# Kernel optimization log

Measured on AMD Instinct MI355X. Metric: run time of the kernel, lower is better.

The kernel has to match this reference:

```python
import jax, jax.numpy as jnp
import numpy as np

DIM = 512
HEADS = 8
HEAD_DIM = DIM // HEADS
SCALE = HEAD_DIM ** -0.5
CPB_HIDDEN = 512
N_CLASSES = 2
LN_EPS = 1e-5


def _layernorm(x, g, b):
    m = jnp.mean(x, axis=-1, keepdims=True)
    v = jnp.var(x, axis=-1, keepdims=True)
    return (x - m) / jnp.sqrt(v + LN_EPS) * g + b


def _coord_attention(x, coords, cpb_w1, cpb_b1, cpb_w2, cpb_b2, qkv_w, qkv_b, proj_w, proj_b):
    B, N, C = x.shape
    qkv = (x @ qkv_w + qkv_b).reshape(B, N, 3, HEADS, HEAD_DIM)
    q, k, v = jnp.moveaxis(qkv, 2, 0)  # each (B, N, H, hd)
    attn = jnp.einsum('bnhd,bmhd->bhnm', q * SCALE, k)  # (B, H, N, N)
    rel = coords[:, :, None, :] - coords[:, None, :, :]  # (B, N, N, 2)
    rel = rel / (jnp.linalg.norm(rel, axis=-1, keepdims=True) + 1e-6)
    bias = jax.nn.relu(rel @ cpb_w1 + cpb_b1) @ cpb_w2 + cpb_b2  # (B, N, N, H)
    attn = jax.nn.softmax(attn + jnp.transpose(bias, (0, 3, 1, 2)), axis=-1)
    out = jnp.einsum('bhnm,bmhd->bnhd', attn, v).reshape(B, N, C)
    return out @ proj_w + proj_b


def setup_inputs() -> dict:
    key = jax.random.key(0)
    ks = iter(jax.random.split(key, 32))
    d = {}
    d['h'] = jax.random.normal(next(ks), (1, 400, 1024), dtype=jnp.float32)
    d['coords'] = jax.random.uniform(next(ks), (1, 400, 2), dtype=jnp.float32) * 1000.0
    def lin(kw, kb, fan_in, fan_out):
        w = jax.random.normal(kw, (fan_in, fan_out), dtype=jnp.float32) / np.sqrt(fan_in)
        b = jax.random.normal(kb, (fan_out,), dtype=jnp.float32) * 0.01
        return w, b
    d['fc1_w'], d['fc1_b'] = lin(next(ks), next(ks), 1024, DIM)
    d['cls_token'] = jax.random.normal(next(ks), (1, 1, DIM), dtype=jnp.float32)
    for p in ('l1', 'l2'):
        d[p + '_norm_g'] = jnp.ones((DIM,), jnp.float32)
        d[p + '_norm_b'] = jnp.zeros((DIM,), jnp.float32)
        d[p + '_cpb_w1'], d[p + '_cpb_b1'] = lin(next(ks), next(ks), 2, CPB_HIDDEN)
        d[p + '_cpb_w2'], d[p + '_cpb_b2'] = lin(next(ks), next(ks), CPB_HIDDEN, HEADS)
        d[p + '_qkv_w'], d[p + '_qkv_b'] = lin(next(ks), next(ks), DIM, 3 * DIM)
        d[p + '_proj_w'], d[p + '_proj_b'] = lin(next(ks), next(ks), DIM, DIM)
    d['norm_g'] = jnp.ones((DIM,), jnp.float32)
    d['norm_b'] = jnp.zeros((DIM,), jnp.float32)
    d['fc2_w'], d['fc2_b'] = lin(next(ks), next(ks), DIM, N_CLASSES)
    return d


def reference(h, coords, fc1_w, fc1_b, cls_token,
              l1_norm_g, l1_norm_b, l1_cpb_w1, l1_cpb_b1, l1_cpb_w2, l1_cpb_b2,
              l1_qkv_w, l1_qkv_b, l1_proj_w, l1_proj_b,
              l2_norm_g, l2_norm_b, l2_cpb_w1, l2_cpb_b1, l2_cpb_w2, l2_cpb_b2,
              l2_qkv_w, l2_qkv_b, l2_proj_w, l2_proj_b,
              norm_g, norm_b, fc2_w, fc2_b):
    B, Np, _ = h.shape
    h = jax.nn.relu(h @ fc1_w + fc1_b)  # (B, N, 512)
    side = int(np.ceil(np.sqrt(Np)))
    add = side * side - Np  # pad bag to a perfect square (wrap-around copy)
    h = jnp.concatenate([h, h[:, :add, :]], axis=1)
    coords = jnp.concatenate([coords, coords[:, :add, :]], axis=1)
    cls = jnp.broadcast_to(cls_token, (B, 1, DIM))
    h = jnp.concatenate([cls, h], axis=1)
    coords = jnp.concatenate([jnp.zeros((B, 1, 2), h.dtype), coords], axis=1)
    h = h + _coord_attention(_layernorm(h, l1_norm_g, l1_norm_b), coords,
                             l1_cpb_w1, l1_cpb_b1, l1_cpb_w2, l1_cpb_b2,
                             l1_qkv_w, l1_qkv_b, l1_proj_w, l1_proj_b)
    h = h + _coord_attention(_layernorm(h, l2_norm_g, l2_norm_b), coords,
                             l2_cpb_w1, l2_cpb_b1, l2_cpb_w2, l2_cpb_b2,
                             l2_qkv_w, l2_qkv_b, l2_proj_w, l2_proj_b)
    h = _layernorm(h, norm_g, norm_b)[:, 0]  # CLS token
    return h @ fc2_w + fc2_b  # (B, n_classes)
```

## Files before the change

### kernel.cpp

```cpp
#include <hip/hip_runtime.h>
#include <math.h>

#define NP 401
#define DIM 512
#define LN_EPS 1e-5f
#define ATT_SCALE 0.125f
#define CPB_M 4096
#define TSTRIDE (CPB_M + 64)
#define PQS (401L * 1536)
#define PKS (401L * 1024)
#define PVS (401L * 512)

template<bool TB, typename LA, typename LB>
__device__ __forceinline__ void gemm64(
    int kBeg, int kEnd, int tid,
    float (*as)[68], float (*bs)[68], float (&acc)[4][4],
    LA&& loadA, LB&& loadB)
{
    float aR[4], bR[4];
    loadA(kBeg, aR);
    loadB(kBeg, bR);
    for (int k0 = kBeg; k0 < kEnd; k0 += 16) {
        const int arow = tid >> 2, aq = tid & 3;
        as[aq * 4 + 0][arow] = aR[0];
        as[aq * 4 + 1][arow] = aR[1];
        as[aq * 4 + 2][arow] = aR[2];
        as[aq * 4 + 3][arow] = aR[3];
        if (!TB) {
            *(float4*)&bs[tid >> 4][(tid & 15) * 4] =
                make_float4(bR[0], bR[1], bR[2], bR[3]);
        } else {
            bs[aq * 4 + 0][arow] = bR[0];
            bs[aq * 4 + 1][arow] = bR[1];
            bs[aq * 4 + 2][arow] = bR[2];
            bs[aq * 4 + 3][arow] = bR[3];
        }
        __syncthreads();
        float nA[4] = {0.f,0.f,0.f,0.f}, nB[4] = {0.f,0.f,0.f,0.f};
        if (k0 + 16 < kEnd) { loadA(k0 + 16, nA); loadB(k0 + 16, nB); }
        const int tx = tid & 15, ty = tid >> 4;
        #pragma unroll
        for (int kk = 0; kk < 16; ++kk) {
            float4 a4 = *(const float4*)&as[kk][ty * 4];
            float4 b4 = *(const float4*)&bs[kk][tx * 4];
            float av[4] = {a4.x, a4.y, a4.z, a4.w};
            float bv[4] = {b4.x, b4.y, b4.z, b4.w};
            #pragma unroll
            for (int r = 0; r < 4; ++r)
                #pragma unroll
                for (int c = 0; c < 4; ++c)
                    acc[r][c] = fmaf(av[r], bv[c], acc[r][c]);
        }
        __syncthreads();
        #pragma unroll
        for (int j = 0; j < 4; ++j) { aR[j] = nA[j]; bR[j] = nB[j]; }
    }
}

template<typename LA, typename LB>
__device__ __forceinline__ void gemm256(
    int kBeg, int kEnd, int tid,
    float (*as)[68], float (*bs)[260], float (&acc)[4][4][4],
    LA&& loadA, LB&& loadB)
{
    float aR[4], bR[4][4];
    loadA(kBeg, aR);
    loadB(kBeg, bR);
    for (int k0 = kBeg; k0 < kEnd; k0 += 16) {
        const int arow = tid >> 2, aq = tid & 3;
        as[aq * 4 + 0][arow] = aR[0];
        as[aq * 4 + 1][arow] = aR[1];
        as[aq * 4 + 2][arow] = aR[2];
        as[aq * 4 + 3][arow] = aR[3];
        {
            const int brow = tid >> 4, bcol = (tid & 15) * 4;
            #pragma unroll
            for (int j = 0; j < 4; ++j)
                *(float4*)&bs[brow][bcol + 64 * j] =
                    make_float4(bR[j][0], bR[j][1], bR[j][2], bR[j][3]);
        }
        __syncthreads();
        float nA[4] = {0.f,0.f,0.f,0.f};
        float nB[4][4] = {};
        if (k0 + 16 < kEnd) { loadA(k0 + 16, nA); loadB(k0 + 16, nB); }
        const int tx = tid & 15, ty = tid >> 4;
        #pragma unroll
        for (int kk = 0; kk < 16; ++kk) {
            float4 a4 = *(const float4*)&as[kk][ty * 4];
            float av[4] = {a4.x, a4.y, a4.z, a4.w};
            #pragma unroll
            for (int j = 0; j < 4; ++j) {
                float4 b4 = *(const float4*)&bs[kk][tx * 4 + 64 * j];
                float bv[4] = {b4.x, b4.y, b4.z, b4.w};
                #pragma unroll
                for (int r = 0; r < 4; ++r)
                    #pragma unroll
                    for (int c = 0; c < 4; ++c)
                        acc[r][j][c] = fmaf(av[r], bv[c], acc[r][j][c]);
            }
        }
        __syncthreads();
        #pragma unroll
        for (int i = 0; i < 4; ++i) aR[i] = nA[i];
        #pragma unroll
        for (int j = 0; j < 4; ++j)
            #pragma unroll
            for (int i = 0; i < 4; ++i) bR[j][i] = nB[j][i];
    }
}

__global__ __launch_bounds__(256) void gemm_split256_kernel(
    const float* __restrict__ A, int lda,
    const float* __restrict__ B, int ldb,
    float* __restrict__ P, int ldc, long slice,
    int M, int K, int skN)
{
    __shared__ float as[16][68], bs[16][260];
    const int tid = threadIdx.x;
    const int m0 = blockIdx.x * 64, n0 = blockIdx.y * 256;
    const int sk = blockIdx.z;
    const int KS = K / skN;
    const int kBeg = sk * KS, kEnd = kBeg + KS;
    float acc[4][4][4] = {};

    auto loadA = [&](int k0, float r[4]) {
        r[0] = r[1] = r[2] = r[3] = 0.f;
        int gm = m0 + (tid >> 2);
        if (gm >= M) return;
        int gk = k0 + (tid & 3) * 4;
        float4 v = *(const float4*)(A + (long)gm * lda + gk);
        r[0]=v.x; r[1]=v.y; r[2]=v.z; r[3]=v.w;
    };
    auto loadB = [&](int k0, float r[4][4]) {
        int gk = k0 + (tid >> 4);
        const float* p = B + (long)gk * ldb + n0 + (tid & 15) * 4;
        #pragma unroll
        for (int j = 0; j < 4; ++j) {
            float4 v = *(const float4*)(p + 64 * j);
            r[j][0]=v.x; r[j][1]=v.y; r[j][2]=v.z; r[j][3]=v.w;
        }
    };
    gemm256(kBeg, kEnd, tid, as, bs, acc, loadA, loadB);

    float* C = P + (long)sk * slice;
    const int tx = tid & 15, ty = tid >> 4;
    #pragma unroll
    for (int r = 0; r < 4; ++r) {
        int m = m0 + ty * 4 + r;
        if (m >= M) continue;
        #pragma unroll
        for (int j = 0; j < 4; ++j)
            *(float4*)&C[(long)m * ldc + n0 + tx * 4 + 64 * j] =
                make_float4(acc[r][j][0], acc[r][j][1],
                            acc[r][j][2], acc[r][j][3]);
    }
}

__global__ __launch_bounds__(256) void flash_kernel(
    const float* __restrict__ Pq,
    const float* __restrict__ qkvb,
    const int* __restrict__ pm, const float* __restrict__ pf,
    const float* __restrict__ T,
    float* __restrict__ PO,
    float* __restrict__ Pml)
{
    __shared__ float as[16][68], bs[16][68];
    __shared__ float pT[64][68];
    __shared__ float vs[64][68];
    const int tid = threadIdx.x;
    const int m0 = blockIdx.x * 64, nb = blockIdx.y, h = blockIdx.z;
    const int n0 = nb * 64;
    float acc[4][4] = {};

    float vreg[4][4];
    {
        int key = n0 + (tid >> 2);
        int d0 = (tid & 3) * 16;
        if (key <= 400) {
            long base = (long)key * 1536 + 1024 + h * 64 + d0;
            #pragma unroll
            for (int i = 0; i < 4; ++i) {
                float4 bb = *(const float4*)(qkvb + 1024 + h * 64 + d0 + i * 4);
                float r0 = bb.x, r1 = bb.y, r2 = bb.z, r3 = bb.w;
                #pragma unroll
                for (int s = 0; s < 8; ++s) {
                    float4 v = *(const float4*)(Pq + (long)s * PQS + base + i * 4);
                    r0 += v.x; r1 += v.y; r2 += v.z; r3 += v.w;
                }
                vreg[i][0] = r0; vreg[i][1] = r1;
                vreg[i][2] = r2; vreg[i][3] = r3;
            }
        } else {
            #pragma unroll
            for (int i = 0; i < 4; ++i)
                vreg[i][0] = vreg[i][1] = vreg[i][2] = vreg[i][3] = 0.f;
        }
    }

    auto loadQ = [&](int k0, float r[4]) {
        int gm = m0 + (tid >> 2);
        if (gm > 400) { r[0]=r[1]=r[2]=r[3]=0.f; return; }
        int gk = k0 + (tid & 3) * 4;
        long base = (long)gm * 1536 + h * 64 + gk;
        float4 bb = *(const float4*)(qkvb + h * 64 + gk);
        r[0] = bb.x; r[1] = bb.y; r[2] = bb.z; r[3] = bb.w;
        #pragma unroll
        for (int s = 0; s < 8; ++s) {
            float4 v = *(const float4*)(Pq + (long)s * PQS + base);
            r[0] += v.x; r[1] += v.y; r[2] += v.z; r[3] += v.w;
        }
    };
    auto loadK = [&](int k0, float r[4]) {
        int gn = n0 + (tid >> 2);
        if (gn > 400) { r[0]=r[1]=r[2]=r[3]=0.f; return; }
        int gk = k0 + (tid & 3) * 4;
        long base = (long)gn * 1536 + 512 + h * 64 + gk;
        float4 bb = *(const float4*)(qkvb + 512 + h * 64 + gk);
        r[0] = bb.x; r[1] = bb.y; r[2] = bb.z; r[3] = bb.w;
        #pragma unroll
        for (int s = 0; s < 8; ++s) {
            float4 v = *(const float4*)(Pq + (long)s * PQS + base);
            r[0] += v.x; r[1] += v.y; r[2] += v.z; r[3] += v.w;
        }
    };
    gemm64<true>(0, 64, tid, as, bs, acc, loadQ, loadK);

    {
        int key = tid >> 2, d0 = (tid & 3) * 16;
        #pragma unroll
        for (int i = 0; i < 4; ++i)
            *(float4*)&vs[key][d0 + i * 4] =
                make_float4(vreg[i][0], vreg[i][1], vreg[i][2], vreg[i][3]);
    }

    const int tx = tid & 15, ty = tid >> 4;
    const float* Tt = T + (long)h * TSTRIDE;
    float p[4][4];
    #pragma unroll
    for (int r = 0; r < 4; ++r) {
        int i = m0 + ty * 4 + r;
        float sv[4];
        #pragma unroll
        for (int c = 0; c < 4; ++c) {
            int j = n0 + tx * 4 + c;
            if (i <= 400 && j <= 400) {
                int id = i * 416 + j;
                int mm = pm[id];
                float fr = pf[id];
                float t0 = Tt[mm], t1 = Tt[mm + 1];
                sv[c] = fmaf(acc[r][c], ATT_SCALE, fmaf(fr, t1 - t0, t0));
            } else {
                sv[c] = -INFINITY;
            }
        }
        float cmax = fmaxf(fmaxf(sv[0], sv[1]), fmaxf(sv[2], sv[3]));
        cmax = fmaxf(cmax, __shfl_xor(cmax, 1));
        cmax = fmaxf(cmax, __shfl_xor(cmax, 2));
        cmax = fmaxf(cmax, __shfl_xor(cmax, 4));
        cmax = fmaxf(cmax, __shfl_xor(cmax, 8));
        const bool rowok = (i <= 400);
        #pragma unroll
        for (int c = 0; c < 4; ++c)
            p[r][c] = rowok ? __expf(sv[c] - cmax) : 0.f;
        float cs = p[r][0] + p[r][1] + p[r][2] + p[r][3];
        cs += __shfl_xor(cs, 1);
        cs += __shfl_xor(cs, 2);
        cs += __shfl_xor(cs, 4);
        cs += __shfl_xor(cs, 8);
        if (tx == 0 && rowok) {
            long o = ((long)(h * 401 + i) * 7 + nb) * 2;
            Pml[o] = cmax;
            Pml[o + 1] = cs;
        }
    }
    #pragma unroll
    for (int c = 0; c < 4; ++c)
        *(float4*)&pT[tx * 4 + c][ty * 4] =
            make_float4(p[0][c], p[1][c], p[2][c], p[3][c]);
    __syncthreads();

    float o[4][4] = {};
    #pragma unroll 16
    for (int kk = 0; kk < 64; ++kk) {
        float4 a4 = *(const float4*)&pT[kk][ty * 4];
        float4 b4 = *(const float4*)&vs[kk][tx * 4];
        float av[4] = {a4.x, a4.y, a4.z, a4.w};
        float bv[4] = {b4.x, b4.y, b4.z, b4.w};
        #pragma unroll
        for (int r = 0; r < 4; ++r)
            #pragma unroll
            for (int c = 0; c < 4; ++c)
                o[r][c] = fmaf(av[r], bv[c], o[r][c]);
    }

    float* C = PO + (long)nb * PVS;
    #pragma unroll
    for (int r = 0; r < 4; ++r) {
        int m = m0 + ty * 4 + r;
        if (m > 400) continue;
        *(float4*)&C[(long)m * 512 + h * 64 + tx * 4] =
            make_float4(o[r][0], o[r][1], o[r][2], o[r][3]);
    }
}

__global__ __launch_bounds__(256) void proj_kernel(
    const float* __restrict__ PO, const float* __restrict__ Pml,
    const float* __restrict__ projw, float* __restrict__ Pp)
{
    __shared__ float as[16][68], bs[16][68];
    __shared__ float wls[64][8];
    const int tid = threadIdx.x;
    const int m0 = blockIdx.x * 64, n0 = blockIdx.y * 64, sk = blockIdx.z;
    const int kBeg = sk * 64, kEnd = kBeg + 64;
    float acc[4][4] = {};

    if (tid < 64) {
        int row = m0 + tid;
        if (row <= 400) {
            const float* q = Pml + ((long)(sk * 401 + row) * 7) * 2;
            float M = -INFINITY;
            #pragma unroll
            for (int c = 0; c < 7; ++c) M = fmaxf(M, q[c * 2]);
            float D = 0.f;
            #pragma unroll
            for (int c = 0; c < 7; ++c) D += q[c * 2 + 1] * __expf(q[c * 2] - M);
            float iD = 1.f / D;
            #pragma unroll
            for (int c = 0; c < 7; ++c) wls[tid][c] = __expf(q[c * 2] - M) * iD;
        } else {
            #pragma unroll
            for (int c = 0; c < 7; ++c) wls[tid][c] = 0.f;
        }
    }
    __syncthreads();

    auto loadA = [&](int k0, float r4[4]) {
        r4[0] = r4[1] = r4[2] = r4[3] = 0.f;
        int lm = tid >> 2, gm = m0 + lm;
        if (gm > 400) return;
        int gk = k0 + (tid & 3) * 4;
        #pragma unroll
        for (int s = 0; s < 7; ++s) {
            float4 v = *(const float4*)(PO + (long)s * PVS + (long)gm * 512 + gk);
            float w = wls[lm][s];
            r4[0] = fmaf(w, v.x, r4[0]);
            r4[1] = fmaf(w, v.y, r4[1]);
            r4[2] = fmaf(w, v.z, r4[2]);
            r4[3] = fmaf(w, v.w, r4[3]);
        }
    };
    auto loadB = [&](int k0, float r[4]) {
        int gk = k0 + (tid >> 4);
        int gn = n0 + (tid & 15) * 4;
        float4 v = *(const float4*)(projw + (long)gk * 512 + gn);
        r[0]=v.x; r[1]=v.y; r[2]=v.z; r[3]=v.w;
    };
    gemm64<false>(kBeg, kEnd, tid, as, bs, acc, loadA, loadB);

    float* C = Pp + (long)sk * PVS;
    const int tx = tid & 15, ty = tid >> 4;
    #pragma unroll
    for (int r = 0; r < 4; ++r) {
        int m = m0 + ty * 4 + r;
        if (m > 400) continue;
        *(float4*)&C[(long)m * 512 + n0 + tx * 4] =
            make_float4(acc[r][0], acc[r][1], acc[r][2], acc[r][3]);
    }
}

__global__ __launch_bounds__(256) void rowfuse_kernel(
    const float* __restrict__ P, long slice, int skN, int rowOff,
    const float* __restrict__ bias, int doRelu,
    const float* __restrict__ resid, const float* __restrict__ cls,
    float* __restrict__ h0,
    const float* __restrict__ g, const float* __restrict__ b,
    float* __restrict__ xln)
{
    const int r = blockIdx.x, t = threadIdx.x;
    float v0, v1;
    if (cls && r == 0) {
        v0 = cls[t]; v1 = cls[t + 256];
    } else {
        const float* p = P + (long)(r - rowOff) * DIM;
        v0 = bias[t]; v1 = bias[t + 256];
        for (int k = 0; k < skN; ++k) {
            v0 += p[(long)k * slice + t];
            v1 += p[(long)k * slice + t + 256];
        }
        if (resid) {
            v0 += resid[(long)r * DIM + t];
            v1 += resid[(long)r * DIM + t + 256];
        }
        if (doRelu) { v0 = fmaxf(v0, 0.f); v1 = fmaxf(v1, 0.f); }
    }
    h0[(long)r * DIM + t] = v0;
    h0[(long)r * DIM + t + 256] = v1;

    float s = v0 + v1, sq = v0 * v0 + v1 * v1;
    #pragma unroll
    for (int off = 32; off > 0; off >>= 1) {
        s += __shfl_down(s, off);
        sq += __shfl_down(sq, off);
    }
    __shared__ float ps[4], pq[4];
    int w = t >> 6, lane = t & 63;
    if (lane == 0) { ps[w] = s; pq[w] = sq; }
    __syncthreads();
    float Sm = ps[0] + ps[1] + ps[2] + ps[3];
    float Q = pq[0] + pq[1] + pq[2] + pq[3];
    float mean = Sm * (1.f / DIM);
    float var = Q * (1.f / DIM) - mean * mean;
    float inv = rsqrtf(var + LN_EPS);
    xln[(long)r * DIM + t]       = (v0 - mean) * inv * g[t] + b[t];
    xln[(long)r * DIM + t + 256] = (v1 - mean) * inv * g[t + 256] + b[t + 256];
}

__global__ __launch_bounds__(256) void cls_decode_kernel(
    const float* __restrict__ xln, const float* __restrict__ qkvw,
    const float* __restrict__ Pkv, const float* __restrict__ qkvb,
    const int* __restrict__ pm, const float* __restrict__ pf,
    const float* __restrict__ T,
    float* __restrict__ cms, float* __restrict__ cpv,
    unsigned* __restrict__ cnt)
{
    const int h = blockIdx.x, c = blockIdx.y, tid = threadIdx.x;
    const int kBeg = c * 64;
    __shared__ float q0[64], scraw[64], p[64], red[4][64], rr[2];

    if (h == 0 && c == 0 && tid == 0) *cnt = 0u;

    {
        int d = tid & 63, w4 = tid >> 6;
        const float* col = qkvw + h * 64 + d;
        float acc = 0.f;
        for (int k = w4 * 128; k < w4 * 128 + 128; ++k)
            acc = fmaf(xln[k], col[(long)k * 1536], acc);
        red[w4][d] = acc;
    }
    __syncthreads();
    if (tid < 64)
        q0[tid] = red[0][tid] + red[1][tid] + red[2][tid] + red[3][tid]
                  + qkvb[h * 64 + tid];
    __syncthreads();

    {
        int k = tid >> 2, q = tid & 3;
        int j = kBeg + k;
        float dot = 0.f;
        if (j < NP) {
            long base = (long)j * 1024 + h * 64 + q * 16;
            #pragma unroll
            for (int d = 0; d < 16; d += 4) {
                float4 x = *(const float4*)(qkvb + 512 + h * 64 + q * 16 + d);
                #pragma unroll
                for (int s = 0; s < 8; ++s) {
                    float4 v = *(const float4*)(Pkv + (long)s * PKS + base + d);
                    x.x += v.x; x.y += v.y; x.z += v.z; x.w += v.w;
                }
                float4 qq = *(const float4*)(q0 + q * 16 + d);
                dot = fmaf(qq.x, x.x, dot);
                dot = fmaf(qq.y, x.y, dot);
                dot = fmaf(qq.z, x.z, dot);
                dot = fmaf(qq.w, x.w, dot);
            }
        }
        dot += __shfl_down(dot, 2);
        dot += __shfl_down(dot, 1);
        if (q == 0) scraw[k] = dot;
    }
    __syncthreads();

    if (tid < 64) {
        int j = kBeg + tid;
        float s;
        if (j < NP) {
            int mm = pm[j];
            float fr = pf[j];
            const float* Tt = T + (long)h * TSTRIDE;
            float t0 = Tt[mm], t1 = Tt[mm + 1];
            s = fmaf(scraw[tid], ATT_SCALE, fmaf(fr, t1 - t0, t0));
        } else {
            s = -INFINITY;
        }
        float m = s;
        #pragma unroll
        for (int off = 32; off > 0; off >>= 1)
            m = fmaxf(m, __shfl_xor(m, off));
        float e = (j < NP) ? __expf(s - m) : 0.f;
        float sum = e;
        #pragma unroll
        for (int off = 32; off > 0; off >>= 1)
            sum += __shfl_xor(sum, off);
        p[tid] = e;
        if (tid == 0) { rr[0] = m; rr[1] = sum; }
    }
    __syncthreads();

    {
        int w = tid >> 6, d = tid & 63;
        float vb = qkvb[1024 + h * 64 + d];
        float acc = 0.f;
        for (int k = w; k < 64; k += 4) {
            int j = kBeg + k;
            if (j >= NP) break;
            long o = (long)j * 1024 + 512 + h * 64 + d;
            float v = vb;
            #pragma unroll
            for (int s = 0; s < 8; ++s) v += Pkv[(long)s * PKS + o];
            acc = fmaf(p[k], v, acc);
        }
        red[w][d] = acc;
    }
    __syncthreads();
    if (tid < 64) {
        cpv[((long)h * 7 + c) * 64 + tid] =
            red[0][tid] + red[1][tid] + red[2][tid] + red[3][tid];
        if (tid == 0) {
            cms[(h * 7 + c) * 2 + 0] = rr[0];
            cms[(h * 7 + c) * 2 + 1] = rr[1];
        }
    }
}

__global__ __launch_bounds__(256) void cls_proj_kernel(
    const float* __restrict__ cms, const float* __restrict__ cpv,
    const float* __restrict__ projw, const float* __restrict__ projb,
    float* __restrict__ proj0,
    const float* __restrict__ h0,
    const float* __restrict__ g, const float* __restrict__ b,
    const float* __restrict__ fc2w, const float* __restrict__ fc2b,
    float* __restrict__ out, unsigned* __restrict__ cnt)
{
    __shared__ float av[512], red[4][64];
    __shared__ int isLast;
    const int bk = blockIdx.x, tid = threadIdx.x;
    for (int d = tid; d < 512; d += 256) {
        int h = d >> 6, dd = d & 63;
        float M = -INFINITY;
        #pragma unroll
        for (int c = 0; c < 7; ++c)
            M = fmaxf(M, cms[(h * 7 + c) * 2]);
        float Sx = 0.f, acc = 0.f;
        #pragma unroll
        for (int c = 0; c < 7; ++c) {
            float e = __expf(cms[(h * 7 + c) * 2] - M);
            Sx += cms[(h * 7 + c) * 2 + 1] * e;
            acc += cpv[((long)h * 7 + c) * 64 + dd] * e;
        }
        av[d] = acc / Sx;
    }
    __syncthreads();
    int gg = tid >> 6, n = bk * 64 + (tid & 63);
    float acc = 0.f;
    for (int k = gg * 128; k < gg * 128 + 128; ++k)
        acc = fmaf(av[k], projw[(long)k * 512 + n], acc);
    red[gg][tid & 63] = acc;
    __syncthreads();
    if (tid < 64)
        proj0[bk * 64 + tid] = red[0][tid] + red[1][tid] + red[2][tid]
                               + red[3][tid] + projb[bk * 64 + tid];

    __threadfence();
    if (tid == 0) isLast = (atomicAdd(cnt, 1u) == 7u);
    __syncthreads();
    if (!isLast) return;
    __threadfence();

    const int t = tid;
    float v0 = h0[t] + proj0[t];
    float v1 = h0[t + 256] + proj0[t + 256];
    float s = v0 + v1, sq = v0 * v0 + v1 * v1;
    #pragma unroll
    for (int off = 32; off > 0; off >>= 1) {
        s += __shfl_down(s, off);
        sq += __shfl_down(sq, off);
    }
    __shared__ float ps[4], pq[4], pc0[4], pc1[4];
    int w = t >> 6, lane = t & 63;
    if (lane == 0) { ps[w] = s; pq[w] = sq; }
    __syncthreads();
    float Sm = ps[0] + ps[1] + ps[2] + ps[3];
    float Q = pq[0] + pq[1] + pq[2] + pq[3];
    float mean = Sm * (1.f / DIM);
    float var = Q * (1.f / DIM) - mean * mean;
    float inv = rsqrtf(var + LN_EPS);
    float n0 = (v0 - mean) * inv * g[t] + b[t];
    float n1 = (v1 - mean) * inv * g[t + 256] + b[t + 256];
    float c0 = n0 * fc2w[t * 2]     + n1 * fc2w[(t + 256) * 2];
    float c1 = n0 * fc2w[t * 2 + 1] + n1 * fc2w[(t + 256) * 2 + 1];
    #pragma unroll
    for (int off = 32; off > 0; off >>= 1) {
        c0 += __shfl_down(c0, off);
        c1 += __shfl_down(c1, off);
    }
    if (lane == 0) { pc0[w] = c0; pc1[w] = c1; }
    __syncthreads();
    if (t == 0) {
        out[0] = pc0[0] + pc0[1] + pc0[2] + pc0[3] + fc2b[0];
        out[1] = pc1[0] + pc1[1] + pc1[2] + pc1[3] + fc2b[1];
    }
}

__global__ __launch_bounds__(256) void mega_kernel(
    const float* __restrict__ hin, const float* __restrict__ fc1_w,
    const float* __restrict__ w1_0, const float* __restrict__ b1_0,
    const float* __restrict__ w2_0, const float* __restrict__ b2_0,
    const float* __restrict__ w1_1, const float* __restrict__ b1_1,
    const float* __restrict__ w2_1, const float* __restrict__ b2_1,
    const float* __restrict__ coords,
    float* __restrict__ Pp, float* __restrict__ T,
    int* __restrict__ pm, float* __restrict__ pf)
{
    __shared__ float smem[5248];
    float (*as)[68]  = (float(*)[68])smem;
    float (*bs)[260] = (float(*)[260])(smem + 1088);
    float (*red)[64][8] = (float(*)[64][8])smem;
    const int bid = blockIdx.x, tid = threadIdx.x;

    if (bid < 224) {
        int sk = bid / 14, rem = bid % 14;
        int m0 = (rem % 7) * 64, n0 = (rem / 7) * 256;
        int kBeg = sk * 64, kEnd = kBeg + 64;
        float acc[4][4][4] = {};
        auto loadA = [&](int k0, float r[4]) {
            r[0]=r[1]=r[2]=r[3]=0.f;
            int gm = m0 + (tid >> 2);
            if (gm >= 400) return;
            int gk = k0 + (tid & 3) * 4;
            float4 v = *(const float4*)(hin + (long)gm * 1024 + gk);
            r[0]=v.x; r[1]=v.y; r[2]=v.z; r[3]=v.w;
        };
        auto loadB = [&](int k0, float r[4][4]) {
            int gk = k0 + (tid >> 4);
            const float* p = fc1_w + (long)gk * 512 + n0 + (tid & 15) * 4;
            #pragma unroll
            for (int j = 0; j < 4; ++j) {
                float4 v = *(const float4*)(p + 64 * j);
                r[j][0]=v.x; r[j][1]=v.y; r[j][2]=v.z; r[j][3]=v.w;
            }
        };
        gemm256(kBeg, kEnd, tid, as, bs, acc, loadA, loadB);
        float* C = Pp + (long)sk * PVS;
        const int tx = tid & 15, ty = tid >> 4;
        #pragma unroll
        for (int r = 0; r < 4; ++r) {
            int m = m0 + ty * 4 + r;
            if (m >= 400) continue;
            #pragma unroll
            for (int j = 0; j < 4; ++j)
                *(float4*)&C[(long)m * 512 + n0 + tx * 4 + 64 * j] =
                    make_float4(acc[r][j][0], acc[r][j][1],
                                acc[r][j][2], acc[r][j][3]);
        }
    } else if (bid < 354) {
        int tb = bid - 224;
        int z = tb / 65, ab = tb % 65;
        const float* w1 = z ? w1_1 : w1_0;
        const float* b1 = z ? b1_1 : b1_0;
        const float* w2 = z ? w2_1 : w2_0;
        const float* b2 = z ? b2_1 : b2_0;
        const int lane = tid & 63, wv = tid >> 6;
        float ca = 0.f, sa = 0.f;
        if (ab != 64) {
            float th = fmaf((float)(ab * 64 + lane),
                            (float)(2.0 * M_PI / CPB_M), -(float)M_PI);
            sincosf(th, &sa, &ca);
        } else if (lane == 0) {
            sincosf((float)M_PI, &sa, &ca);
        }
        float a8[8] = {};
        const int kbeg = wv * 128;
        #pragma unroll 4
        for (int k = kbeg; k < kbeg + 128; ++k) {
            float hk = fmaxf(fmaf(ca, w1[k],
                                  fmaf(sa, w1[512 + k], b1[k])), 0.f);
            #pragma unroll
            for (int h2 = 0; h2 < 8; ++h2)
                a8[h2] = fmaf(hk, w2[k * 8 + h2], a8[h2]);
        }
        #pragma unroll
        for (int h2 = 0; h2 < 8; ++h2) red[wv][lane][h2] = a8[h2];
        __syncthreads();
        if (tid < 64) {
            int aidx = ab * 64 + tid;
            if (aidx <= CPB_M + 1) {
                #pragma unroll
                for (int h2 = 0; h2 < 8; ++h2)
                    T[(long)(z * 8 + h2) * TSTRIDE + aidx] =
                        red[0][tid][h2] + red[1][tid][h2] +
                        red[2][tid][h2] + red[3][tid][h2] + b2[h2];
            }
        }
    } else {
        int p = (bid - 354) * 256 + tid;
        if (p < NP * NP) {
            int i = p / NP, j = p - i * NP;
            float xi = (i == 0) ? 0.f : coords[(i - 1) * 2];
            float yi = (i == 0) ? 0.f : coords[(i - 1) * 2 + 1];
            float xj = (j == 0) ? 0.f : coords[(j - 1) * 2];
            float yj = (j == 0) ? 0.f : coords[(j - 1) * 2 + 1];
            float rx = xi - xj, ry = yi - yj;
            int mm; float fr;
            if (rx == 0.f && ry == 0.f) {
                mm = CPB_M + 1; fr = 0.f;
            } else {
                float x = (atan2f(ry, rx) + 3.14159265358979f)
                          * (float)(CPB_M / (2.0 * M_PI));
                int mi = (int)x;
                fr = x - (float)mi;
                mm = (mi >= CPB_M) ? mi - CPB_M : mi;
            }
            pm[i * 416 + j] = mm;
            pf[i * 416 + j] = fr;
        }
    }
}

extern "C" void kernel_launch(void* const* d_in, const int* in_sizes, int n_in,
                              void* d_out, int out_size, void* d_ws, size_t ws_size,
                              hipStream_t stream)
{
    const float* coords = (const float*)d_in[1];
    float* ws = (float*)d_ws;
    float* h0   = ws;                    ws += 401L * 512;
    float* xln  = ws;                    ws += 401L * 512;
    float* PO   = ws;                    ws += 7L * PVS;
    float* T    = ws;                    ws += 16L * TSTRIDE;
    int*   pm   = (int*)ws;              ws += 401L * 416;
    float* pf   = ws;                    ws += 401L * 416;
    float* Pq   = ws;                    ws += 8L * PQS;
    float* Pp   = ws;                    ws += 16L * PVS;
    float* proj0 = ws;                   ws += 512;
    float* cms  = ws;                    ws += 8L * 7 * 2;
    float* cpv  = ws;                    ws += 8L * 7 * 64;
    float* Pml  = ws;                    ws += 8L * 401 * 7 * 2;
    unsigned* cnt = (unsigned*)ws;       ws += 16;

    mega_kernel<<<983, 256, 0, stream>>>(
        (const float*)d_in[0], (const float*)d_in[2],
        (const float*)d_in[7],  (const float*)d_in[8],
        (const float*)d_in[9],  (const float*)d_in[10],
        (const float*)d_in[17], (const float*)d_in[18],
        (const float*)d_in[19], (const float*)d_in[20],
        coords, Pp, T, pm, pf);

    rowfuse_kernel<<<401, 256, 0, stream>>>(
        Pp, PVS, 16, 1, (const float*)d_in[3], 1, nullptr,
        (const float*)d_in[4], h0,
        (const float*)d_in[5], (const float*)d_in[6], xln);

    gemm_split256_kernel<<<dim3(7, 6, 8), 256, 0, stream>>>(
        xln, 512, (const float*)d_in[11], 1536, Pq, 1536, PQS,
        401, 512, 8);
    flash_kernel<<<dim3(7, 7, 8), 256, 0, stream>>>(
        Pq, (const float*)d_in[12], pm, pf, T, PO, Pml);
    proj_kernel<<<dim3(7, 8, 8), 256, 0, stream>>>(
        PO, Pml, (const float*)d_in[13], Pp);
    rowfuse_kernel<<<401, 256, 0, stream>>>(
        Pp, PVS, 8, 0, (const float*)d_in[14], 0, h0, nullptr, h0,
        (const float*)d_in[15], (const float*)d_in[16], xln);

    gemm_split256_kernel<<<dim3(7, 4, 8), 256, 0, stream>>>(
        xln, 512, (const float*)d_in[21] + 512, 1536, Pq, 1024, PKS,
        401, 512, 8);
    cls_decode_kernel<<<dim3(8, 7), 256, 0, stream>>>(
        xln, (const float*)d_in[21], Pq, (const float*)d_in[22],
        pm, pf, T + 8L * TSTRIDE, cms, cpv, cnt);
    cls_proj_kernel<<<8, 256, 0, stream>>>(
        cms, cpv, (const float*)d_in[23], (const float*)d_in[24], proj0,
        h0, (const float*)d_in[25], (const float*)d_in[26],
        (const float*)d_in[27], (const float*)d_in[28], (float*)d_out, cnt);
}
```

Baseline: 266.2 us.

## Cut split-K depth for QKV GEMMs and move attention combine to its own kernel

The layer-1 QKV GEMM now uses 64x128 tiles with 2-way split-K instead of 64x256 tiles with 8-way split-K. Flash attention therefore sums only 2 partial slices when loading Q, K and V, where it used to sum 8, and it does this in every block that reads them. The layer-2 K/V GEMM switches to 64x64 tiles with 4-way split-K, and cls_decode reads 4 partials instead of 8. The flash-decoding merge of partial outputs moves out of proj_kernel into a new combine_kernel that writes a normalized attention buffer. The cost is one extra launch and one extra intermediate buffer, plus GEMMs with longer per-block K loops.

```diff
diff --git a/kernel.cpp b/kernel.cpp
--- a/kernel.cpp
+++ b/kernel.cpp
@@ -58,6 +58,586 @@
 }
 
 template<typename LA, typename LB>
+__device__ __forceinline__ void gemm128(
+    int kBeg, int kEnd, int tid,
+    float (*as)[68], float (*bs)[132], float (&acc)[4][2][4],
+    LA&& loadA, LB&& loadB)
+{
+    float aR[4], bR[2][4];
+    loadA(kBeg, aR);
+    loadB(kBeg, bR);
+    for (int k0 = kBeg; k0 < kEnd; k0 += 16) {
+        const int arow = tid >> 2, aq = tid & 3;
+        as[aq * 4 + 0][arow] = aR[0];
+        as[aq * 4 + 1][arow] = aR[1];
+        as[aq * 4 + 2][arow] = aR[2];
+        as[aq * 4 + 3][arow] = aR[3];
+        {
+            const int brow = tid >> 4, bcol = (tid & 15) * 4;
+            *(float4*)&bs[brow][bcol] =
+                make_float4(bR[0][0], bR[0][1], bR[0][2], bR[0][3]);
+            *(float4*)&bs[brow][bcol + 64] =
+                make_float4(bR[1][0], bR[1][1], bR[1][2], bR[1][3]);
+        }
+        __syncthreads();
+        float nA[4] = {0.f,0.f,0.f,0.f};
+        float nB[2][4] = {};
+        if (k0 + 16 < kEnd) { loadA(k0 + 16, nA); loadB(k0 + 16, nB); }
+        const int tx = tid & 15, ty = tid >> 4;
+        #pragma unroll
+        for (int kk = 0; kk < 16; ++kk) {
+            float4 a4 = *(const float4*)&as[kk][ty * 4];
+            float av[4] = {a4.x, a4.y, a4.z, a4.w};
+            #pragma unroll
+            for (int j = 0; j < 2; ++j) {
+                float4 b4 = *(const float4*)&bs[kk][tx * 4 + 64 * j];
+                float bv[4] = {b4.x, b4.y, b4.z, b4.w};
+                #pragma unroll
+                for (int r = 0; r < 4; ++r)
+                    #pragma unroll
+                    for (int c = 0; c < 4; ++c)
+                        acc[r][j][c] = fmaf(av[r], bv[c], acc[r][j][c]);
+            }
+        }
+        __syncthreads();
+        #pragma unroll
+        for (int i = 0; i < 4; ++i) aR[i] = nA[i];
+        #pragma unroll
+        for (int j = 0; j < 2; ++j)
+            #pragma unroll
+            for (int i = 0; i < 4; ++i) bR[j][i] = nB[j][i];
+    }
+}
+
+__global__ __launch_bounds__(256) void gemm_split128_kernel(
+    const float* __restrict__ A, int lda,
+    const float* __restrict__ B, int ldb,
+    float* __restrict__ P, int ldc, long slice,
+    int M, int K, int skN)
+{
+    __shared__ float as[16][68], bs[16][132];
+    const int tid = threadIdx.x;
+    const int m0 = blockIdx.x * 64, n0 = blockIdx.y * 128;
+    const int sk = blockIdx.z;
+    const int KS = K / skN;
+    const int kBeg = sk * KS, kEnd = kBeg + KS;
+    float acc[4][2][4] = {};
+
+    auto loadA = [&](int k0, float r[4]) {
+        r[0] = r[1] = r[2] = r[3] = 0.f;
+        int gm = m0 + (tid >> 2);
+        if (gm >= M) return;
+        int gk = k0 + (tid & 3) * 4;
+        float4 v = *(const float4*)(A + (long)gm * lda + gk);
+        r[0]=v.x; r[1]=v.y; r[2]=v.z; r[3]=v.w;
+    };
+    auto loadB = [&](int k0, float r[2][4]) {
+        int gk = k0 + (tid >> 4);
+        const float* p = B + (long)gk * ldb + n0 + (tid & 15) * 4;
+        #pragma unroll
+        for (int j = 0; j < 2; ++j) {
+            float4 v = *(const float4*)(p + 64 * j);
+            r[j][0]=v.x; r[j][1]=v.y; r[j][2]=v.z; r[j][3]=v.w;
+        }
+    };
+    gemm128(kBeg, kEnd, tid, as, bs, acc, loadA, loadB);
+
+    float* C = P + (long)sk * slice;
+    const int tx = tid & 15, ty = tid >> 4;
+    #pragma unroll
+    for (int r = 0; r < 4; ++r) {
+        int m = m0 + ty * 4 + r;
+        if (m >= M) continue;
+        #pragma unroll
+        for (int j = 0; j < 2; ++j)
+            *(float4*)&C[(long)m * ldc + n0 + tx * 4 + 64 * j] =
+                make_float4(acc[r][j][0], acc[r][j][1],
+                            acc[r][j][2], acc[r][j][3]);
+    }
+}
+
+__global__ __launch_bounds__(256) void gemm_split_kernel(
+    const float* __restrict__ A, int lda,
+    const float* __restrict__ B, int ldb,
+    float* __restrict__ P, int ldc, long slice,
+    int M, int K, int skN)
+{
+    __shared__ float as[16][68], bs[16][68];
+    const int tid = threadIdx.x;
+    const int m0 = blockIdx.x * 64, n0 = blockIdx.y * 64;
+    const int sk = blockIdx.z;
+    const int KS = K / skN;
+    const int kBeg = sk * KS, kEnd = kBeg + KS;
+    float acc[4][4] = {};
+
+    auto loadA = [&](int k0, float r[4]) {
+        r[0] = r[1] = r[2] = r[3] = 0.f;
+        int gm = m0 + (tid >> 2);
+        if (gm >= M) return;
+        int gk = k0 + (tid & 3) * 4;
+        float4 v = *(const float4*)(A + (long)gm * lda + gk);
+        r[0]=v.x; r[1]=v.y; r[2]=v.z; r[3]=v.w;
+    };
+    auto loadB = [&](int k0, float r[4]) {
+        int gk = k0 + (tid >> 4);
+        int gn = n0 + (tid & 15) * 4;
+        float4 v = *(const float4*)(B + (long)gk * ldb + gn);
+        r[0]=v.x; r[1]=v.y; r[2]=v.z; r[3]=v.w;
+    };
+    gemm64<false>(kBeg, kEnd, tid, as, bs, acc, loadA, loadB);
+
+    float* C = P + (long)sk * slice;
+    const int tx = tid & 15, ty = tid >> 4;
+    #pragma unroll
+    for (int r = 0; r < 4; ++r) {
+        int m = m0 + ty * 4 + r;
+        if (m >= M) continue;
+        *(float4*)&C[(long)m * ldc + n0 + tx * 4] =
+            make_float4(acc[r][0], acc[r][1], acc[r][2], acc[r][3]);
+    }
+}
+
+__global__ __launch_bounds__(256) void flash_kernel(
+    const float* __restrict__ Pq,
+    const float* __restrict__ qkvb,
+    const int* __restrict__ pm, const float* __restrict__ pf,
+    const float* __restrict__ T,
+    float* __restrict__ PO,
+    float* __restrict__ Pml)
+{
+    __shared__ float as[16][68], bs[16][68];
+    __shared__ float pT[64][68];
+    __shared__ float vs[64][68];
+    const int tid = threadIdx.x;
+    const int m0 = blockIdx.x * 64, nb = blockIdx.y, h = blockIdx.z;
+    const int n0 = nb * 64;
+    float acc[4][4] = {};
+
+    float vreg[4][4];
+    {
+        int key = n0 + (tid >> 2);
+        int d0 = (tid & 3) * 16;
+        if (key <= 400) {
+            long base = (long)key * 1536 + 1024 + h * 64 + d0;
+            #pragma unroll
+            for (int i = 0; i < 4; ++i) {
+                float4 v0 = *(const float4*)(Pq + base + i * 4);
+                float4 v1 = *(const float4*)(Pq + PQS + base + i * 4);
+                float4 bb = *(const float4*)(qkvb + 1024 + h * 64 + d0 + i * 4);
+                vreg[i][0] = v0.x + v1.x + bb.x;
+                vreg[i][1] = v0.y + v1.y + bb.y;
+                vreg[i][2] = v0.z + v1.z + bb.z;
+                vreg[i][3] = v0.w + v1.w + bb.w;
+            }
+        } else {
+            #pragma unroll
+            for (int i = 0; i < 4; ++i)
+                vreg[i][0] = vreg[i][1] = vreg[i][2] = vreg[i][3] = 0.f;
+        }
+    }
+
+    auto loadQ = [&](int k0, float r[4]) {
+        int gm = m0 + (tid >> 2);
+        if (gm > 400) { r[0]=r[1]=r[2]=r[3]=0.f; return; }
+        int gk = k0 + (tid & 3) * 4;
+        long base = (long)gm * 1536 + h * 64 + gk;
+        float4 v0 = *(const float4*)(Pq + base);
+        float4 v1 = *(const float4*)(Pq + PQS + base);
+        float4 bb = *(const float4*)(qkvb + h * 64 + gk);
+        r[0] = v0.x + v1.x + bb.x;
+        r[1] = v0.y + v1.y + bb.y;
+        r[2] = v0.z + v1.z + bb.z;
+        r[3] = v0.w + v1.w + bb.w;
+    };
+    auto loadK = [&](int k0, float r[4]) {
+        int gn = n0 + (tid >> 2);
+        if (gn > 400) { r[0]=r[1]=r[2]=r[3]=0.f; return; }
+        int gk = k0 + (tid & 3) * 4;
+        long base = (long)gn * 1536 + 512 + h * 64 + gk;
+        float4 v0 = *(const float4*)(Pq + base);
+        float4 v1 = *(const float4*)(Pq + PQS + base);
+        float4 bb = *(const float4*)(qkvb + 512 + h * 64 + gk);
+        r[0] = v0.x + v1.x + bb.x;
+        r[1] = v0.y + v1.y + bb.y;
+        r[2] = v0.z + v1.z + bb.z;
+        r[3] = v0.w + v1.w + bb.w;
+    };
+    gemm64<true>(0, 64, tid, as, bs, acc, loadQ, loadK);
+
+    {
+        int key = tid >> 2, d0 = (tid & 3) * 16;
+        #pragma unroll
+        for (int i = 0; i < 4; ++i)
+            *(float4*)&vs[key][d0 + i * 4] =
+                make_float4(vreg[i][0], vreg[i][1], vreg[i][2], vreg[i][3]);
+    }
+
+    const int tx = tid & 15, ty = tid >> 4;
+    const float* Tt = T + (long)h * TSTRIDE;
+    float p[4][4];
+    #pragma unroll
+    for (int r = 0; r < 4; ++r) {
+        int i = m0 + ty * 4 + r;
+        float sv[4];
+        #pragma unroll
+        for (int c = 0; c < 4; ++c) {
+            int j = n0 + tx * 4 + c;
+            if (i <= 400 && j <= 400) {
+                int id = i * 416 + j;
+                int mm = pm[id];
+                float fr = pf[id];
+                float t0 = Tt[mm], t1 = Tt[mm + 1];
+                sv[c] = fmaf(acc[r][c], ATT_SCALE, fmaf(fr, t1 - t0, t0));
+            } else {
+                sv[c] = -INFINITY;
+            }
+        }
+        float cmax = fmaxf(fmaxf(sv[0], sv[1]), fmaxf(sv[2], sv[3]));
+        cmax = fmaxf(cmax, __shfl_xor(cmax, 1));
+        cmax = fmaxf(cmax, __shfl_xor(cmax, 2));
+        cmax = fmaxf(cmax, __shfl_xor(cmax, 4));
+        cmax = fmaxf(cmax, __shfl_xor(cmax, 8));
+        const bool rowok = (i <= 400);
+        #pragma unroll
+        for (int c = 0; c < 4; ++c)
+            p[r][c] = rowok ? __expf(sv[c] - cmax) : 0.f;
+        float cs = p[r][0] + p[r][1] + p[r][2] + p[r][3];
+        cs += __shfl_xor(cs, 1);
+        cs += __shfl_xor(cs, 2);
+        cs += __shfl_xor(cs, 4);
+        cs += __shfl_xor(cs, 8);
+        if (tx == 0 && rowok) {
+            long o = ((long)(h * 401 + i) * 7 + nb) * 2;
+            Pml[o] = cmax;
+            Pml[o + 1] = cs;
+        }
+    }
+    #pragma unroll
+    for (int c = 0; c < 4; ++c)
+        *(float4*)&pT[tx * 4 + c][ty * 4] =
+            make_float4(p[0][c], p[1][c], p[2][c], p[3][c]);
+    __syncthreads();
+
+    float o[4][4] = {};
+    #pragma unroll 16
+    for (int kk = 0; kk < 64; ++kk) {
+        float4 a4 = *(const float4*)&pT[kk][ty * 4];
+        float4 b4 = *(const float4*)&vs[kk][tx * 4];
+        float av[4] = {a4.x, a4.y, a4.z, a4.w};
+        float bv[4] = {b4.x, b4.y, b4.z, b4.w};
+        #pragma unroll
+        for (int r = 0; r < 4; ++r)
+            #pragma unroll
+            for (int c = 0; c < 4; ++c)
+                o[r][c] = fmaf(av[r], bv[c], o[r][c]);
+    }
+
+    float* C = PO + (long)nb * PVS;
+    #pragma unroll
+    for (int r = 0; r < 4; ++r) {
+        int m = m0 + ty * 4 + r;
+        if (m > 400) continue;
+        *(float4*)&C[(long)m * 512 + h * 64 + tx * 4] =
+            make_float4(o[r][0], o[r][1], o[r][2], o[r][3]);
+    }
+}
+
+__global__ __launch_bounds__(256) void combine_kernel(
+    const float* __restrict__ PO, const float* __restrict__ Pml,
+    float* __restrict__ att)
+{
+    const int r = blockIdx.x, t = threadIdx.x;
+    #pragma unroll
+    for (int half = 0; half < 2; ++half) {
+        int d = t + half * 256;
+        int h = d >> 6;
+        const float* q = Pml + ((long)(h * 401 + r) * 7) * 2;
+        float M = -INFINITY;
+        #pragma unroll
+        for (int c = 0; c < 7; ++c) M = fmaxf(M, q[c * 2]);
+        float D = 0.f;
+        #pragma unroll
+        for (int c = 0; c < 7; ++c) D += q[c * 2 + 1] * __expf(q[c * 2] - M);
+        float acc = 0.f;
+        #pragma unroll
+        for (int s = 0; s < 7; ++s)
+            acc = fmaf(__expf(q[s * 2] - M),
+                       PO[(long)s * PVS + (long)r * 512 + d], acc);
+        att[(long)r * 512 + d] = acc / D;
+    }
+}
+
+__global__ __launch_bounds__(256) void proj_kernel(
+    const float* __restrict__ att,
+    const float* __restrict__ projw, float* __restrict__ Pp)
+{
+    __shared__ float as[16][68], bs[16][68];
+    const int tid = threadIdx.x;
+    const int m0 = blockIdx.x * 64, n0 = blockIdx.y * 64, sk = blockIdx.z;
+    const int kBeg = sk * 64, kEnd = kBeg + 64;
+    float acc[4][4] = {};
+
+    auto loadA = [&](int k0, float r[4]) {
+        r[0] = r[1] = r[2] = r[3] = 0.f;
+        int gm = m0 + (tid >> 2);
+        if (gm > 400) return;
+        int gk = k0 + (tid & 3) * 4;
+        float4 v = *(const float4*)(att + (long)gm * 512 + gk);
+        r[0]=v.x; r[1]=v.y; r[2]=v.z; r[3]=v.w;
+    };
+    auto loadB = [&](int k0, float r[4]) {
+        int gk = k0 + (tid >> 4);
+        int gn = n0 + (tid & 15) * 4;
+        float4 v = *(const float4*)(projw + (long)gk * 512 + gn);
+        r[0]=v.x; r[1]=v.y; r[2]=v.z; r[3]=v.w;
+    };
+    gemm64<false>(kBeg, kEnd, tid, as, bs, acc, loadA, loadB);
+
+    float* C = Pp + (long)sk * PVS;
+    const int tx = tid & 15, ty = tid >> 4;
+    #pragma unroll
+    for (int r = 0; r < 4; ++r) {
+        int m = m0 + ty * 4 + r;
+        if (m > 400) continue;
+        *(float4*)&C[(long)m * 512 + n0 + tx * 4] =
+            make_float4(acc[r][0], acc[r][1], acc[r][2], acc[r][3]);
+    }
+}
+
+__global__ __launch_bounds__(256) void rowfuse_kernel(
+    const float* __restrict__ P, long slice, int skN, int rowOff,
+    const float* __restrict__ bias, int doRelu,
+    const float* __restrict__ resid, const float* __restrict__ cls,
+    float* __restrict__ h0,
+    const float* __restrict__ g, const float* __restrict__ b,
+    float* __restrict__ xln)
+{
+    const int r = blockIdx.x, t = threadIdx.x;
+    float v0, v1;
+    if (cls && r == 0) {
+        v0 = cls[t]; v1 = cls[t + 256];
+    } else {
+        const float* p = P + (long)(r - rowOff) * DIM;
+        v0 = bias[t]; v1 = bias[t + 256];
+        for (int k = 0; k < skN; ++k) {
+            v0 += p[(long)k * slice + t];
+            v1 += p[(long)k * slice + t + 256];
+        }
+        if (resid) {
+            v0 += resid[(long)r * DIM + t];
+            v1 += resid[(long)r * DIM + t + 256];
+        }
+        if (doRelu) { v0 = fmaxf(v0, 0.f); v1 = fmaxf(v1, 0.f); }
+    }
+    h0[(long)r * DIM + t] = v0;
+    h0[(long)r * DIM + t + 256] = v1;
+
+    float s = v0 + v1, sq = v0 * v0 + v1 * v1;
+    #pragma unroll
+    for (int off = 32; off > 0; off >>= 1) {
+        s += __shfl_down(s, off);
+        sq += __shfl_down(sq, off);
+    }
+    __shared__ float ps[4], pq[4];
+    int w = t >> 6, lane = t & 63;
+    if (lane == 0) { ps[w] = s; pq[w] = sq; }
+    __syncthreads();
+    float Sm = ps[0] + ps[1] + ps[2] + ps[3];
+    float Q = pq[0] + pq[1] + pq[2] + pq[3];
+    float mean = Sm * (1.f / DIM);
+    float var = Q * (1.f / DIM) - mean * mean;
+    float inv = rsqrtf(var + LN_EPS);
+    xln[(long)r * DIM + t]       = (v0 - mean) * inv * g[t] + b[t];
+    xln[(long)r * DIM + t + 256] = (v1 - mean) * inv * g[t + 256] + b[t + 256];
+}
+
+__global__ __launch_bounds__(256) void cls_decode_kernel(
+    const float* __restrict__ xln, const float* __restrict__ qkvw,
+    const float* __restrict__ Pkv, const float* __restrict__ qkvb,
+    const int* __restrict__ pm, const float* __restrict__ pf,
+    const float* __restrict__ T,
+    float* __restrict__ cms, float* __restrict__ cpv,
+    unsigned* __restrict__ cnt)
+{
+    const int h = blockIdx.x, c = blockIdx.y, tid = threadIdx.x;
+    const int kBeg = c * 64;
+    __shared__ float q0[64], scraw[64], p[64], red[4][64], rr[2];
+
+    if (h == 0 && c == 0 && tid == 0) *cnt = 0u;
+
+    {
+        int d = tid & 63, w4 = tid >> 6;
+        const float* col = qkvw + h * 64 + d;
+        float acc = 0.f;
+        for (int k = w4 * 128; k < w4 * 128 + 128; ++k)
+            acc = fmaf(xln[k], col[(long)k * 1536], acc);
+        red[w4][d] = acc;
+    }
+    __syncthreads();
+    if (tid < 64)
+        q0[tid] = red[0][tid] + red[1][tid] + red[2][tid] + red[3][tid]
+                  + qkvb[h * 64 + tid];
+    __syncthreads();
+
+    {
+        int k = tid >> 2, q = tid & 3;
+        int j = kBeg + k;
+        float dot = 0.f;
+        if (j < NP) {
+            long base = (long)j * 1024 + h * 64 + q * 16;
+            #pragma unroll
+            for (int d = 0; d < 16; d += 4) {
+                float4 x = *(const float4*)(qkvb + 512 + h * 64 + q * 16 + d);
+                #pragma unroll
+                for (int s = 0; s < 4; ++s) {
+                    float4 v = *(const float4*)(Pkv + (long)s * PKS + base + d);
+                    x.x += v.x; x.y += v.y; x.z += v.z; x.w += v.w;
+                }
+                float4 qq = *(const float4*)(q0 + q * 16 + d);
+                dot = fmaf(qq.x, x.x, dot);
+                dot = fmaf(qq.y, x.y, dot);
+                dot = fmaf(qq.z, x.z, dot);
+                dot = fmaf(qq.w, x.w, dot);
+            }
+        }
+        dot += __shfl_down(dot, 2);
+        dot += __shfl_down(dot, 1);
+        if (q == 0) scraw[k] = dot;
+    }
+    __syncthreads();
+
+    if (tid < 64) {
+        int j = kBeg + tid;
+        float s;
+        if (j < NP) {
+            int mm = pm[j];
+            float fr = pf[j];
+            const float* Tt = T + (long)h * TSTRIDE;
+            float t0 = Tt[mm], t1 = Tt[mm + 1];
+            s = fmaf(scraw[tid], ATT_SCALE, fmaf(fr, t1 - t0, t0));
+        } else {
+            s = -INFINITY;
+        }
+        float m = s;
+        #pragma unroll
+        for (int off = 32; off > 0; off >>= 1)
+            m = fmaxf(m, __shfl_xor(m, off));
+        float e = (j < NP) ? __expf(s - m) : 0.f;
+        float sum = e;
+        #pragma unroll
+        for (int off = 32; off > 0; off >>= 1)
+            sum += __shfl_xor(sum, off);
+        p[tid] = e;
+        if (tid == 0) { rr[0] = m; rr[1] = sum; }
+    }
+    __syncthreads();
+
+    {
+        int w = tid >> 6, d = tid & 63;
+        float vb = qkvb[1024 + h * 64 + d];
+        float acc = 0.f;
+        for (int k = w; k < 64; k += 4) {
+            int j = kBeg + k;
+            if (j >= NP) break;
+            long o = (long)j * 1024 + 512 + h * 64 + d;
+            float v = vb;
+            #pragma unroll
+            for (int s = 0; s < 4; ++s) v += Pkv[(long)s * PKS + o];
+            acc = fmaf(p[k], v, acc);
+        }
+        red[w][d] = acc;
+    }
+    __syncthreads();
+    if (tid < 64) {
+        cpv[((long)h * 7 + c) * 64 + tid] =
+            red[0][tid] + red[1][tid] + red[2][tid] + red[3][tid];
+        if (tid == 0) {
+            cms[(h * 7 + c) * 2 + 0] = rr[0];
+            cms[(h * 7 + c) * 2 + 1] = rr[1];
+        }
+    }
+}
+
+__global__ __launch_bounds__(256) void cls_proj_kernel(
+    const float* __restrict__ cms, const float* __restrict__ cpv,
+    const float* __restrict__ projw, const float* __restrict__ projb,
+    float* __restrict__ proj0,
+    const float* __restrict__ h0,
+    const float* __restrict__ g, const float* __restrict__ b,
+    const float* __restrict__ fc2w, const float* __restrict__ fc2b,
+    float* __restrict__ out, unsigned* __restrict__ cnt)
+{
+    __shared__ float av[512], red[4][64];
+    __shared__ int isLast;
+    const int bk = blockIdx.x, tid = threadIdx.x;
+    for (int d = tid; d < 512; d += 256) {
+        int h = d >> 6, dd = d & 63;
+        float M = -INFINITY;
+        #pragma unroll
+        for (int c = 0; c < 7; ++c)
+            M = fmaxf(M, cms[(h * 7 + c) * 2]);
+        float Sx = 0.f, acc = 0.f;
+        #pragma unroll
+        for (int c = 0; c < 7; ++c) {
+            float e = __expf(cms[(h * 7 + c) * 2] - M);
+            Sx += cms[(h * 7 + c) * 2 + 1] * e;
+            acc += cpv[((long)h * 7 + c) * 64 + dd] * e;
+        }
+        av[d] = acc / Sx;
+    }
+    __syncthreads();
+    int gg = tid >> 6, n = bk * 64 + (tid & 63);
+    float acc = 0.f;
+    for (int k = gg * 128; k < gg * 128 + 128; ++k)
+        acc = fmaf(av[k], projw[(long)k * 512 + n], acc);
+    red[gg][tid & 63] = acc;
+    __syncthreads();
+    if (tid < 64)
+        proj0[bk * 64 + tid] = red[0][tid] + red[1][tid] + red[2][tid]
+                               + red[3][tid] + projb[bk * 64 + tid];
+
+    __threadfence();
+    if (tid == 0) isLast = (atomicAdd(cnt, 1u) == 7u);
+    __syncthreads();
+    if (!isLast) return;
+    __threadfence();
+
+    const int t = tid;
+    float v0 = h0[t] + proj0[t];
+    float v1 = h0[t + 256] + proj0[t + 256];
+    float s = v0 + v1, sq = v0 * v0 + v1 * v1;
+    #pragma unroll
+    for (int off = 32; off > 0; off >>= 1) {
+        s += __shfl_down(s, off);
+        sq += __shfl_down(sq, off);
+    }
+    __shared__ float ps[4], pq[4], pc0[4], pc1[4];
+    int w = t >> 6, lane = t & 63;
+    if (lane == 0) { ps[w] = s; pq[w] = sq; }
+    __syncthreads();
+    float Sm = ps[0] + ps[1] + ps[2] + ps[3];
+    float Q = pq[0] + pq[1] + pq[2] + pq[3];
+    float mean = Sm * (1.f / DIM);
+    float var = Q * (1.f / DIM) - mean * mean;
+    float inv = rsqrtf(var + LN_EPS);
+    float n0 = (v0 - mean) * inv * g[t] + b[t];
+    float n1 = (v1 - mean) * inv * g[t + 256] + b[t + 256];
+    float c0 = n0 * fc2w[t * 2]     + n1 * fc2w[(t + 256) * 2];
+    float c1 = n0 * fc2w[t * 2 + 1] + n1 * fc2w[(t + 256) * 2 + 1];
+    #pragma unroll
+    for (int off = 32; off > 0; off >>= 1) {
+        c0 += __shfl_down(c0, off);
+        c1 += __shfl_down(c1, off);
+    }
+    if (lane == 0) { pc0[w] = c0; pc1[w] = c1; }
+    __syncthreads();
+    if (t == 0) {
+        out[0] = pc0[0] + pc0[1] + pc0[2] + pc0[3] + fc2b[0];
+        out[1] = pc1[0] + pc1[1] + pc1[2] + pc1[3] + fc2b[1];
+    }
+}
+
+template<typename LA, typename LB>
 __device__ __forceinline__ void gemm256(
     int kBeg, int kEnd, int tid,
     float (*as)[68], float (*bs)[260], float (&acc)[4][4][4],
@@ -106,498 +686,6 @@
         for (int j = 0; j < 4; ++j)
             #pragma unroll
             for (int i = 0; i < 4; ++i) bR[j][i] = nB[j][i];
-    }
-}
-
-__global__ __launch_bounds__(256) void gemm_split256_kernel(
-    const float* __restrict__ A, int lda,
-    const float* __restrict__ B, int ldb,
-    float* __restrict__ P, int ldc, long slice,
-    int M, int K, int skN)
-{
-    __shared__ float as[16][68], bs[16][260];
-    const int tid = threadIdx.x;
-    const int m0 = blockIdx.x * 64, n0 = blockIdx.y * 256;
-    const int sk = blockIdx.z;
-    const int KS = K / skN;
-    const int kBeg = sk * KS, kEnd = kBeg + KS;
-    float acc[4][4][4] = {};
-
-    auto loadA = [&](int k0, float r[4]) {
-        r[0] = r[1] = r[2] = r[3] = 0.f;
-        int gm = m0 + (tid >> 2);
-        if (gm >= M) return;
-        int gk = k0 + (tid & 3) * 4;
-        float4 v = *(const float4*)(A + (long)gm * lda + gk);
-        r[0]=v.x; r[1]=v.y; r[2]=v.z; r[3]=v.w;
-    };
-    auto loadB = [&](int k0, float r[4][4]) {
-        int gk = k0 + (tid >> 4);
-        const float* p = B + (long)gk * ldb + n0 + (tid & 15) * 4;
-        #pragma unroll
-        for (int j = 0; j < 4; ++j) {
-            float4 v = *(const float4*)(p + 64 * j);
-            r[j][0]=v.x; r[j][1]=v.y; r[j][2]=v.z; r[j][3]=v.w;
-        }
-    };
-    gemm256(kBeg, kEnd, tid, as, bs, acc, loadA, loadB);
-
-    float* C = P + (long)sk * slice;
-    const int tx = tid & 15, ty = tid >> 4;
-    #pragma unroll
-    for (int r = 0; r < 4; ++r) {
-        int m = m0 + ty * 4 + r;
-        if (m >= M) continue;
-        #pragma unroll
-        for (int j = 0; j < 4; ++j)
-            *(float4*)&C[(long)m * ldc + n0 + tx * 4 + 64 * j] =
-                make_float4(acc[r][j][0], acc[r][j][1],
-                            acc[r][j][2], acc[r][j][3]);
-    }
-}
-
-__global__ __launch_bounds__(256) void flash_kernel(
-    const float* __restrict__ Pq,
-    const float* __restrict__ qkvb,
-    const int* __restrict__ pm, const float* __restrict__ pf,
-    const float* __restrict__ T,
-    float* __restrict__ PO,
-    float* __restrict__ Pml)
-{
-    __shared__ float as[16][68], bs[16][68];
-    __shared__ float pT[64][68];
-    __shared__ float vs[64][68];
-    const int tid = threadIdx.x;
-    const int m0 = blockIdx.x * 64, nb = blockIdx.y, h = blockIdx.z;
-    const int n0 = nb * 64;
-    float acc[4][4] = {};
-
-    float vreg[4][4];
-    {
-        int key = n0 + (tid >> 2);
-        int d0 = (tid & 3) * 16;
-        if (key <= 400) {
-            long base = (long)key * 1536 + 1024 + h * 64 + d0;
-            #pragma unroll
-            for (int i = 0; i < 4; ++i) {
-                float4 bb = *(const float4*)(qkvb + 1024 + h * 64 + d0 + i * 4);
-                float r0 = bb.x, r1 = bb.y, r2 = bb.z, r3 = bb.w;
-                #pragma unroll
-                for (int s = 0; s < 8; ++s) {
-                    float4 v = *(const float4*)(Pq + (long)s * PQS + base + i * 4);
-                    r0 += v.x; r1 += v.y; r2 += v.z; r3 += v.w;
-                }
-                vreg[i][0] = r0; vreg[i][1] = r1;
-                vreg[i][2] = r2; vreg[i][3] = r3;
-            }
-        } else {
-            #pragma unroll
-            for (int i = 0; i < 4; ++i)
-                vreg[i][0] = vreg[i][1] = vreg[i][2] = vreg[i][3] = 0.f;
-        }
-    }
-
-    auto loadQ = [&](int k0, float r[4]) {
-        int gm = m0 + (tid >> 2);
-        if (gm > 400) { r[0]=r[1]=r[2]=r[3]=0.f; return; }
-        int gk = k0 + (tid & 3) * 4;
-        long base = (long)gm * 1536 + h * 64 + gk;
-        float4 bb = *(const float4*)(qkvb + h * 64 + gk);
-        r[0] = bb.x; r[1] = bb.y; r[2] = bb.z; r[3] = bb.w;
-        #pragma unroll
-        for (int s = 0; s < 8; ++s) {
-            float4 v = *(const float4*)(Pq + (long)s * PQS + base);
-            r[0] += v.x; r[1] += v.y; r[2] += v.z; r[3] += v.w;
-        }
-    };
-    auto loadK = [&](int k0, float r[4]) {
-        int gn = n0 + (tid >> 2);
-        if (gn > 400) { r[0]=r[1]=r[2]=r[3]=0.f; return; }
-        int gk = k0 + (tid & 3) * 4;
-        long base = (long)gn * 1536 + 512 + h * 64 + gk;
-        float4 bb = *(const float4*)(qkvb + 512 + h * 64 + gk);
-        r[0] = bb.x; r[1] = bb.y; r[2] = bb.z; r[3] = bb.w;
-        #pragma unroll
-        for (int s = 0; s < 8; ++s) {
-            float4 v = *(const float4*)(Pq + (long)s * PQS + base);
-            r[0] += v.x; r[1] += v.y; r[2] += v.z; r[3] += v.w;
-        }
-    };
-    gemm64<true>(0, 64, tid, as, bs, acc, loadQ, loadK);
-
-    {
-        int key = tid >> 2, d0 = (tid & 3) * 16;
-        #pragma unroll
-        for (int i = 0; i < 4; ++i)
-            *(float4*)&vs[key][d0 + i * 4] =
-                make_float4(vreg[i][0], vreg[i][1], vreg[i][2], vreg[i][3]);
-    }
-
-    const int tx = tid & 15, ty = tid >> 4;
-    const float* Tt = T + (long)h * TSTRIDE;
-    float p[4][4];
-    #pragma unroll
-    for (int r = 0; r < 4; ++r) {
-        int i = m0 + ty * 4 + r;
-        float sv[4];
-        #pragma unroll
-        for (int c = 0; c < 4; ++c) {
-            int j = n0 + tx * 4 + c;
-            if (i <= 400 && j <= 400) {
-                int id = i * 416 + j;
-                int mm = pm[id];
-                float fr = pf[id];
-                float t0 = Tt[mm], t1 = Tt[mm + 1];
-                sv[c] = fmaf(acc[r][c], ATT_SCALE, fmaf(fr, t1 - t0, t0));
-            } else {
-                sv[c] = -INFINITY;
-            }
-        }
-        float cmax = fmaxf(fmaxf(sv[0], sv[1]), fmaxf(sv[2], sv[3]));
-        cmax = fmaxf(cmax, __shfl_xor(cmax, 1));
-        cmax = fmaxf(cmax, __shfl_xor(cmax, 2));
-        cmax = fmaxf(cmax, __shfl_xor(cmax, 4));
-        cmax = fmaxf(cmax, __shfl_xor(cmax, 8));
-        const bool rowok = (i <= 400);
-        #pragma unroll
-        for (int c = 0; c < 4; ++c)
-            p[r][c] = rowok ? __expf(sv[c] - cmax) : 0.f;
-        float cs = p[r][0] + p[r][1] + p[r][2] + p[r][3];
-        cs += __shfl_xor(cs, 1);
-        cs += __shfl_xor(cs, 2);
-        cs += __shfl_xor(cs, 4);
-        cs += __shfl_xor(cs, 8);
-        if (tx == 0 && rowok) {
-            long o = ((long)(h * 401 + i) * 7 + nb) * 2;
-            Pml[o] = cmax;
-            Pml[o + 1] = cs;
-        }
-    }
-    #pragma unroll
-    for (int c = 0; c < 4; ++c)
-        *(float4*)&pT[tx * 4 + c][ty * 4] =
-            make_float4(p[0][c], p[1][c], p[2][c], p[3][c]);
-    __syncthreads();
-
-    float o[4][4] = {};
-    #pragma unroll 16
-    for (int kk = 0; kk < 64; ++kk) {
-        float4 a4 = *(const float4*)&pT[kk][ty * 4];
-        float4 b4 = *(const float4*)&vs[kk][tx * 4];
-        float av[4] = {a4.x, a4.y, a4.z, a4.w};
-        float bv[4] = {b4.x, b4.y, b4.z, b4.w};
-        #pragma unroll
-        for (int r = 0; r < 4; ++r)
-            #pragma unroll
-            for (int c = 0; c < 4; ++c)
-                o[r][c] = fmaf(av[r], bv[c], o[r][c]);
-    }
-
-    float* C = PO + (long)nb * PVS;
-    #pragma unroll
-    for (int r = 0; r < 4; ++r) {
-        int m = m0 + ty * 4 + r;
-        if (m > 400) continue;
-        *(float4*)&C[(long)m * 512 + h * 64 + tx * 4] =
-            make_float4(o[r][0], o[r][1], o[r][2], o[r][3]);
-    }
-}
-
-__global__ __launch_bounds__(256) void proj_kernel(
-    const float* __restrict__ PO, const float* __restrict__ Pml,
-    const float* __restrict__ projw, float* __restrict__ Pp)
-{
-    __shared__ float as[16][68], bs[16][68];
-    __shared__ float wls[64][8];
-    const int tid = threadIdx.x;
-    const int m0 = blockIdx.x * 64, n0 = blockIdx.y * 64, sk = blockIdx.z;
-    const int kBeg = sk * 64, kEnd = kBeg + 64;
-    float acc[4][4] = {};
-
-    if (tid < 64) {
-        int row = m0 + tid;
-        if (row <= 400) {
-            const float* q = Pml + ((long)(sk * 401 + row) * 7) * 2;
-            float M = -INFINITY;
-            #pragma unroll
-            for (int c = 0; c < 7; ++c) M = fmaxf(M, q[c * 2]);
-            float D = 0.f;
-            #pragma unroll
-            for (int c = 0; c < 7; ++c) D += q[c * 2 + 1] * __expf(q[c * 2] - M);
-            float iD = 1.f / D;
-            #pragma unroll
-            for (int c = 0; c < 7; ++c) wls[tid][c] = __expf(q[c * 2] - M) * iD;
-        } else {
-            #pragma unroll
-            for (int c = 0; c < 7; ++c) wls[tid][c] = 0.f;
-        }
-    }
-    __syncthreads();
-
-    auto loadA = [&](int k0, float r4[4]) {
-        r4[0] = r4[1] = r4[2] = r4[3] = 0.f;
-        int lm = tid >> 2, gm = m0 + lm;
-        if (gm > 400) return;
-        int gk = k0 + (tid & 3) * 4;
-        #pragma unroll
-        for (int s = 0; s < 7; ++s) {
-            float4 v = *(const float4*)(PO + (long)s * PVS + (long)gm * 512 + gk);
-            float w = wls[lm][s];
-            r4[0] = fmaf(w, v.x, r4[0]);
-            r4[1] = fmaf(w, v.y, r4[1]);
-            r4[2] = fmaf(w, v.z, r4[2]);
-            r4[3] = fmaf(w, v.w, r4[3]);
-        }
-    };
-    auto loadB = [&](int k0, float r[4]) {
-        int gk = k0 + (tid >> 4);
-        int gn = n0 + (tid & 15) * 4;
-        float4 v = *(const float4*)(projw + (long)gk * 512 + gn);
-        r[0]=v.x; r[1]=v.y; r[2]=v.z; r[3]=v.w;
-    };
-    gemm64<false>(kBeg, kEnd, tid, as, bs, acc, loadA, loadB);
-
-    float* C = Pp + (long)sk * PVS;
-    const int tx = tid & 15, ty = tid >> 4;
-    #pragma unroll
-    for (int r = 0; r < 4; ++r) {
-        int m = m0 + ty * 4 + r;
-        if (m > 400) continue;
-        *(float4*)&C[(long)m * 512 + n0 + tx * 4] =
-            make_float4(acc[r][0], acc[r][1], acc[r][2], acc[r][3]);
-    }
-}
-
-__global__ __launch_bounds__(256) void rowfuse_kernel(
-    const float* __restrict__ P, long slice, int skN, int rowOff,
-    const float* __restrict__ bias, int doRelu,
-    const float* __restrict__ resid, const float* __restrict__ cls,
-    float* __restrict__ h0,
-    const float* __restrict__ g, const float* __restrict__ b,
-    float* __restrict__ xln)
-{
-    const int r = blockIdx.x, t = threadIdx.x;
-    float v0, v1;
-    if (cls && r == 0) {
-        v0 = cls[t]; v1 = cls[t + 256];
-    } else {
-        const float* p = P + (long)(r - rowOff) * DIM;
-        v0 = bias[t]; v1 = bias[t + 256];
-        for (int k = 0; k < skN; ++k) {
-            v0 += p[(long)k * slice + t];
-            v1 += p[(long)k * slice + t + 256];
-        }
-        if (resid) {
-            v0 += resid[(long)r * DIM + t];
-            v1 += resid[(long)r * DIM + t + 256];
-        }
-        if (doRelu) { v0 = fmaxf(v0, 0.f); v1 = fmaxf(v1, 0.f); }
-    }
-    h0[(long)r * DIM + t] = v0;
-    h0[(long)r * DIM + t + 256] = v1;
-
-    float s = v0 + v1, sq = v0 * v0 + v1 * v1;
-    #pragma unroll
-    for (int off = 32; off > 0; off >>= 1) {
-        s += __shfl_down(s, off);
-        sq += __shfl_down(sq, off);
-    }
-    __shared__ float ps[4], pq[4];
-    int w = t >> 6, lane = t & 63;
-    if (lane == 0) { ps[w] = s; pq[w] = sq; }
-    __syncthreads();
-    float Sm = ps[0] + ps[1] + ps[2] + ps[3];
-    float Q = pq[0] + pq[1] + pq[2] + pq[3];
-    float mean = Sm * (1.f / DIM);
-    float var = Q * (1.f / DIM) - mean * mean;
-    float inv = rsqrtf(var + LN_EPS);
-    xln[(long)r * DIM + t]       = (v0 - mean) * inv * g[t] + b[t];
-    xln[(long)r * DIM + t + 256] = (v1 - mean) * inv * g[t + 256] + b[t + 256];
-}
-
-__global__ __launch_bounds__(256) void cls_decode_kernel(
-    const float* __restrict__ xln, const float* __restrict__ qkvw,
-    const float* __restrict__ Pkv, const float* __restrict__ qkvb,
-    const int* __restrict__ pm, const float* __restrict__ pf,
-    const float* __restrict__ T,
-    float* __restrict__ cms, float* __restrict__ cpv,
-    unsigned* __restrict__ cnt)
-{
-    const int h = blockIdx.x, c = blockIdx.y, tid = threadIdx.x;
-    const int kBeg = c * 64;
-    __shared__ float q0[64], scraw[64], p[64], red[4][64], rr[2];
-
-    if (h == 0 && c == 0 && tid == 0) *cnt = 0u;
-
-    {
-        int d = tid & 63, w4 = tid >> 6;
-        const float* col = qkvw + h * 64 + d;
-        float acc = 0.f;
-        for (int k = w4 * 128; k < w4 * 128 + 128; ++k)
-            acc = fmaf(xln[k], col[(long)k * 1536], acc);
-        red[w4][d] = acc;
-    }
-    __syncthreads();
-    if (tid < 64)
-        q0[tid] = red[0][tid] + red[1][tid] + red[2][tid] + red[3][tid]
-                  + qkvb[h * 64 + tid];
-    __syncthreads();
-
-    {
-        int k = tid >> 2, q = tid & 3;
-        int j = kBeg + k;
-        float dot = 0.f;
-        if (j < NP) {
-            long base = (long)j * 1024 + h * 64 + q * 16;
-            #pragma unroll
-            for (int d = 0; d < 16; d += 4) {
-                float4 x = *(const float4*)(qkvb + 512 + h * 64 + q * 16 + d);
-                #pragma unroll
-                for (int s = 0; s < 8; ++s) {
-                    float4 v = *(const float4*)(Pkv + (long)s * PKS + base + d);
-                    x.x += v.x; x.y += v.y; x.z += v.z; x.w += v.w;
-                }
-                float4 qq = *(const float4*)(q0 + q * 16 + d);
-                dot = fmaf(qq.x, x.x, dot);
-                dot = fmaf(qq.y, x.y, dot);
-                dot = fmaf(qq.z, x.z, dot);
-                dot = fmaf(qq.w, x.w, dot);
-            }
-        }
-        dot += __shfl_down(dot, 2);
-        dot += __shfl_down(dot, 1);
-        if (q == 0) scraw[k] = dot;
-    }
-    __syncthreads();
-
-    if (tid < 64) {
-        int j = kBeg + tid;
-        float s;
-        if (j < NP) {
-            int mm = pm[j];
-            float fr = pf[j];
-            const float* Tt = T + (long)h * TSTRIDE;
-            float t0 = Tt[mm], t1 = Tt[mm + 1];
-            s = fmaf(scraw[tid], ATT_SCALE, fmaf(fr, t1 - t0, t0));
-        } else {
-            s = -INFINITY;
-        }
-        float m = s;
-        #pragma unroll
-        for (int off = 32; off > 0; off >>= 1)
-            m = fmaxf(m, __shfl_xor(m, off));
-        float e = (j < NP) ? __expf(s - m) : 0.f;
-        float sum = e;
-        #pragma unroll
-        for (int off = 32; off > 0; off >>= 1)
-            sum += __shfl_xor(sum, off);
-        p[tid] = e;
-        if (tid == 0) { rr[0] = m; rr[1] = sum; }
-    }
-    __syncthreads();
-
-    {
-        int w = tid >> 6, d = tid & 63;
-        float vb = qkvb[1024 + h * 64 + d];
-        float acc = 0.f;
-        for (int k = w; k < 64; k += 4) {
-            int j = kBeg + k;
-            if (j >= NP) break;
-            long o = (long)j * 1024 + 512 + h * 64 + d;
-            float v = vb;
-            #pragma unroll
-            for (int s = 0; s < 8; ++s) v += Pkv[(long)s * PKS + o];
-            acc = fmaf(p[k], v, acc);
-        }
-        red[w][d] = acc;
-    }
-    __syncthreads();
-    if (tid < 64) {
-        cpv[((long)h * 7 + c) * 64 + tid] =
-            red[0][tid] + red[1][tid] + red[2][tid] + red[3][tid];
-        if (tid == 0) {
-            cms[(h * 7 + c) * 2 + 0] = rr[0];
-            cms[(h * 7 + c) * 2 + 1] = rr[1];
-        }
-    }
-}
-
-__global__ __launch_bounds__(256) void cls_proj_kernel(
-    const float* __restrict__ cms, const float* __restrict__ cpv,
-    const float* __restrict__ projw, const float* __restrict__ projb,
-    float* __restrict__ proj0,
-    const float* __restrict__ h0,
-    const float* __restrict__ g, const float* __restrict__ b,
-    const float* __restrict__ fc2w, const float* __restrict__ fc2b,
-    float* __restrict__ out, unsigned* __restrict__ cnt)
-{
-    __shared__ float av[512], red[4][64];
-    __shared__ int isLast;
-    const int bk = blockIdx.x, tid = threadIdx.x;
-    for (int d = tid; d < 512; d += 256) {
-        int h = d >> 6, dd = d & 63;
-        float M = -INFINITY;
-        #pragma unroll
-        for (int c = 0; c < 7; ++c)
-            M = fmaxf(M, cms[(h * 7 + c) * 2]);
-        float Sx = 0.f, acc = 0.f;
-        #pragma unroll
-        for (int c = 0; c < 7; ++c) {
-            float e = __expf(cms[(h * 7 + c) * 2] - M);
-            Sx += cms[(h * 7 + c) * 2 + 1] * e;
-            acc += cpv[((long)h * 7 + c) * 64 + dd] * e;
-        }
-        av[d] = acc / Sx;
-    }
-    __syncthreads();
-    int gg = tid >> 6, n = bk * 64 + (tid & 63);
-    float acc = 0.f;
-    for (int k = gg * 128; k < gg * 128 + 128; ++k)
-        acc = fmaf(av[k], projw[(long)k * 512 + n], acc);
-    red[gg][tid & 63] = acc;
-    __syncthreads();
-    if (tid < 64)
-        proj0[bk * 64 + tid] = red[0][tid] + red[1][tid] + red[2][tid]
-                               + red[3][tid] + projb[bk * 64 + tid];
-
-    __threadfence();
-    if (tid == 0) isLast = (atomicAdd(cnt, 1u) == 7u);
-    __syncthreads();
-    if (!isLast) return;
-    __threadfence();
-
-    const int t = tid;
-    float v0 = h0[t] + proj0[t];
-    float v1 = h0[t + 256] + proj0[t + 256];
-    float s = v0 + v1, sq = v0 * v0 + v1 * v1;
-    #pragma unroll
-    for (int off = 32; off > 0; off >>= 1) {
-        s += __shfl_down(s, off);
-        sq += __shfl_down(sq, off);
-    }
-    __shared__ float ps[4], pq[4], pc0[4], pc1[4];
-    int w = t >> 6, lane = t & 63;
-    if (lane == 0) { ps[w] = s; pq[w] = sq; }
-    __syncthreads();
-    float Sm = ps[0] + ps[1] + ps[2] + ps[3];
-    float Q = pq[0] + pq[1] + pq[2] + pq[3];
-    float mean = Sm * (1.f / DIM);
-    float var = Q * (1.f / DIM) - mean * mean;
-    float inv = rsqrtf(var + LN_EPS);
-    float n0 = (v0 - mean) * inv * g[t] + b[t];
-    float n1 = (v1 - mean) * inv * g[t + 256] + b[t + 256];
-    float c0 = n0 * fc2w[t * 2]     + n1 * fc2w[(t + 256) * 2];
-    float c1 = n0 * fc2w[t * 2 + 1] + n1 * fc2w[(t + 256) * 2 + 1];
-    #pragma unroll
-    for (int off = 32; off > 0; off >>= 1) {
-        c0 += __shfl_down(c0, off);
-        c1 += __shfl_down(c1, off);
-    }
-    if (lane == 0) { pc0[w] = c0; pc1[w] = c1; }
-    __syncthreads();
-    if (t == 0) {
-        out[0] = pc0[0] + pc0[1] + pc0[2] + pc0[3] + fc2b[0];
-        out[1] = pc1[0] + pc1[1] + pc1[2] + pc1[3] + fc2b[1];
     }
 }
 
@@ -724,11 +812,12 @@
     float* ws = (float*)d_ws;
     float* h0   = ws;                    ws += 401L * 512;
     float* xln  = ws;                    ws += 401L * 512;
+    float* att  = ws;                    ws += 401L * 512;
     float* PO   = ws;                    ws += 7L * PVS;
     float* T    = ws;                    ws += 16L * TSTRIDE;
     int*   pm   = (int*)ws;              ws += 401L * 416;
     float* pf   = ws;                    ws += 401L * 416;
-    float* Pq   = ws;                    ws += 8L * PQS;
+    float* Pq   = ws;                    ws += 4L * PKS;
     float* Pp   = ws;                    ws += 16L * PVS;
     float* proj0 = ws;                   ws += 512;
     float* cms  = ws;                    ws += 8L * 7 * 2;
@@ -749,20 +838,21 @@
         (const float*)d_in[4], h0,
         (const float*)d_in[5], (const float*)d_in[6], xln);
 
-    gemm_split256_kernel<<<dim3(7, 6, 8), 256, 0, stream>>>(
+    gemm_split128_kernel<<<dim3(7, 12, 2), 256, 0, stream>>>(
         xln, 512, (const float*)d_in[11], 1536, Pq, 1536, PQS,
-        401, 512, 8);
+        401, 512, 2);
     flash_kernel<<<dim3(7, 7, 8), 256, 0, stream>>>(
         Pq, (const float*)d_in[12], pm, pf, T, PO, Pml);
+    combine_kernel<<<401, 256, 0, stream>>>(PO, Pml, att);
     proj_kernel<<<dim3(7, 8, 8), 256, 0, stream>>>(
-        PO, Pml, (const float*)d_in[13], Pp);
+        att, (const float*)d_in[13], Pp);
     rowfuse_kernel<<<401, 256, 0, stream>>>(
         Pp, PVS, 8, 0, (const float*)d_in[14], 0, h0, nullptr, h0,
         (const float*)d_in[15], (const float*)d_in[16], xln);
 
-    gemm_split256_kernel<<<dim3(7, 4, 8), 256, 0, stream>>>(
+    gemm_split_kernel<<<dim3(7, 16, 4), 256, 0, stream>>>(
         xln, 512, (const float*)d_in[21] + 512, 1536, Pq, 1024, PKS,
-        401, 512, 8);
+        401, 512, 4);
     cls_decode_kernel<<<dim3(8, 7), 256, 0, stream>>>(
         xln, (const float*)d_in[21], Pq, (const float*)d_in[22],
         pm, pf, T + 8L * TSTRIDE, cms, cpv, cnt);
```

Result: faster. 238.0 us (-10.6%).
